# Kernel optimization log

Hardware: AMD Instinct MI355X
Metric: run time of the kernel (lower is better)

Reference implementation:

```python
import jax, jax.numpy as jnp
import numpy as np

N_NODES = 20000
N_EDGES = 200000
C = 64             # channel multiplicity (hidden_irreps = 64x0e + 64x1o)
LMAX = 3
NLM = (LMAX + 1) ** 2   # 16 spherical-harmonic components
NUM_ELEM = 10
R_DIM = 8          # radial embedding out dim
MLP_H = 64
AVG_NEI = 10.0
L_OF_LM = np.repeat(np.arange(LMAX + 1), 2 * np.arange(LMAX + 1) + 1)  # [16] l index per lm slot


def setup_inputs() -> dict:
    key = jax.random.key(0)
    k = jax.random.split(key, 16)
    f32 = jnp.float32
    elems = jax.random.randint(k[0], (N_NODES,), 0, NUM_ELEM)
    one_hot = jax.nn.one_hot(elems, NUM_ELEM, dtype=f32)
    node_features = jax.random.normal(k[1], (N_NODES, C), dtype=f32)
    angular_embedding = jax.random.normal(k[2], (N_EDGES, NLM), dtype=f32)
    radial_embedding = jax.random.normal(k[3], (N_EDGES, R_DIM), dtype=f32)
    edge_index = jax.random.randint(k[4], (2, N_EDGES), 0, N_NODES)

    def w(kk, shape, fan_in):  # e3nn-style 1/sqrt(fan_in) normalization baked into init
        return jax.random.normal(kk, shape, dtype=f32) / float(np.sqrt(fan_in))

    W_up = w(k[5], (C, C), C)
    W_mlp1 = w(k[6], (R_DIM, MLP_H), R_DIM)
    W_mlp2 = w(k[7], (MLP_H, MLP_H), MLP_H)
    W_mlp3 = w(k[8], (MLP_H, MLP_H), MLP_H)
    W_mlp4 = w(k[9], (MLP_H, (LMAX + 1) * C), MLP_H)
    W_lin = w(k[10], (LMAX + 1, C, C), C)
    W_skip = w(k[11], (C, NUM_ELEM, C), C * NUM_ELEM)
    W_c0 = jax.random.normal(k[12], (NUM_ELEM, C), dtype=f32)
    W_c1 = jax.random.normal(k[13], (NUM_ELEM, C), dtype=f32)
    W_p0 = w(k[14], (C, C), C)
    W_p1 = w(k[15], (C, C), C)
    return dict(node_features=node_features, one_hot=one_hot,
                angular_embedding=angular_embedding, radial_embedding=radial_embedding,
                W_up=W_up, W_mlp1=W_mlp1, W_mlp2=W_mlp2, W_mlp3=W_mlp3, W_mlp4=W_mlp4,
                W_lin=W_lin, W_skip=W_skip, W_c0=W_c0, W_c1=W_c1, W_p0=W_p0, W_p1=W_p1,
                edge_index=edge_index)


def reference(node_features, one_hot, angular_embedding, radial_embedding,
              W_up, W_mlp1, W_mlp2, W_mlp3, W_mlp4, W_lin, W_skip,
              W_c0, W_c1, W_p0, W_p1, edge_index):
    sender, receiver = edge_index[0], edge_index[1]
    n = node_features.shape[0]
    # ---- interaction block (RealAgnosticResidual; node feats are pure scalars 64x0e) ----
    x = node_features @ W_up                                    # linear_up [N,C]
    h = jax.nn.silu(radial_embedding @ W_mlp1)                  # radial MLP -> per-edge TP weights
    h = jax.nn.silu(h @ W_mlp2)
    h = jax.nn.silu(h @ W_mlp3)
    tp_w = (h @ W_mlp4).reshape(-1, LMAX + 1, C)                # [E,4,C] (one weight per l path, uvu)
    w_lm = tp_w[:, L_OF_LM, :]                                  # [E,16,C]
    # uvu tensor product of 0e node feats with spherical harmonics (CG trivial for 0e x l -> l)
    msg = x[sender][:, None, :] * angular_embedding[:, :, None] * w_lm   # [E,16,C]
    agg = jax.ops.segment_sum(msg, receiver, num_segments=n) / AVG_NEI   # scatter-sum [N,16,C]
    feats = jnp.einsum('nmc,mck->nmk', agg, W_lin[L_OF_LM])     # per-l channel-mixing linear [N,16,C]
    # residual skip FCTP(64x0e, 10x0e -> hidden): only the 0e block is connected
    sc0 = jnp.einsum('nc,na,cak->nk', node_features, one_hot, W_skip)    # [N,C]
    # ---- equivariant product basis block (correlation = 1) ----
    wn0 = one_hot @ W_c0                                        # element-dependent weights [N,C]
    wn1 = one_hot @ W_c1
    f0 = feats[:, 0, :] * wn0                                   # l=0 output [N,C]
    f1 = feats[:, 1:4, :] * wn1[:, None, :]                     # l=1 output [N,3,C]
    out0 = f0 @ W_p0 + sc0                                      # [N,C]
    out1 = jnp.einsum('nmc,ck->nmk', f1, W_p1)                  # [N,3,C] (sc 1o block is zero)
    # flatten to e3nn channel-major irreps layout -> node_env [N, C*(1+3)]
    return jnp.concatenate([out0, jnp.swapaxes(out1, 1, 2).reshape(n, -1)], axis=-1)
```

## Files before the change

### kernel.cpp

```cpp
#include <hip/hip_runtime.h>

typedef __attribute__((ext_vector_type(8))) short s16x8;
typedef __attribute__((ext_vector_type(4))) float f32x4;

__device__ inline float bf2f(ushort u) {
    union { unsigned int i; float f; } v; v.i = ((unsigned)u) << 16; return v.f;
}
__device__ inline float u2f(unsigned u) {
    union { unsigned int i; float f; } v; v.i = u; return v.f;
}
__device__ inline ushort f2bf(float f) {
    union { float f; unsigned int i; } v; v.f = f;
    unsigned r = v.i + 0x7FFFu + ((v.i >> 16) & 1u);
    return (ushort)(r >> 16);
}
__device__ inline unsigned cvt_pk(float lo, float hi) {
    unsigned d;
    asm("v_cvt_pk_bf16_f32 %0, %1, %2" : "=v"(d) : "v"(lo), "v"(hi));
    return d;
}
__device__ inline float silu_f(float x) {
    float e;
    asm("v_exp_f32 %0, %1" : "=v"(e) : "v"(x * -1.44269504f));
    float d = 1.f + e, r;
    asm("v_rcp_f32 %0, %1" : "=v"(r) : "v"(d));
    return x * r;
}

__global__ __launch_bounds__(256) void prep_up_kernel(
    const float* __restrict__ nf, const float* __restrict__ W_up,
    ushort* __restrict__ x_ws,
    const float* __restrict__ W1, const float* __restrict__ W2,
    const float* __restrict__ W3, const float* __restrict__ W4,
    const float* __restrict__ W_lin, const float* __restrict__ Wp0,
    const float* __restrict__ Wp1, const float* __restrict__ W_skip,
    ushort* __restrict__ wimg, int* __restrict__ counts, int N) {
    __shared__ float sW[64 * 64];
    __shared__ float sNf[32][64];
    int tid = threadIdx.x;
    int nub = N / 32;
    if ((int)blockIdx.x < nub) {
        size_t n0 = (size_t)blockIdx.x * 32;
        for (int i = tid; i < 4096; i += 256) sW[i] = W_up[i];
        for (int i = tid; i < 2048; i += 256) {
            int r = i >> 6, c = i & 63;
            sNf[r][c] = nf[(n0 + r) * 64 + c];
        }
        __syncthreads();
        int r = tid >> 3, k0 = (tid & 7) * 8;
        float acc[8] = {0, 0, 0, 0, 0, 0, 0, 0};
        #pragma unroll 4
        for (int c = 0; c < 64; ++c) {
            float v = sNf[r][c];
            const float* wr = &sW[c * 64 + k0];
            #pragma unroll
            for (int j = 0; j < 8; ++j) acc[j] += v * wr[j];
        }
        uint4 val;
        val.x = cvt_pk(acc[0], acc[1]);
        val.y = cvt_pk(acc[2], acc[3]);
        val.z = cvt_pk(acc[4], acc[5]);
        val.w = cvt_pk(acc[6], acc[7]);
        *(uint4*)(x_ws + (n0 + r) * 64 + k0) = val;
        return;
    }
    int idx = ((int)blockIdx.x - nub) * 256 + tid;
    if (idx < N) counts[idx] = 0;
    if (idx < 4096) {
        int m = idx >> 6, k = idx & 63;
        int dst = m * 64 + ((((k >> 3) ^ (m & 7))) << 3) + (k & 7);
        wimg[dst] = (k < 8) ? f2bf(W1[k * 64 + m]) : (ushort)0;
    } else if (idx < 8192) {
        int i = idx - 4096;
        int m = i >> 6, k = i & 63;
        int dst = 4096 + m * 64 + ((((k >> 3) ^ (m & 7))) << 3) + (k & 7);
        wimg[dst] = f2bf(W2[k * 64 + m]);
    } else if (idx < 12288) {
        int i = idx - 8192;
        int m = i >> 6, k = i & 63;
        int dst = 8192 + m * 64 + ((((k >> 3) ^ (m & 7))) << 3) + (k & 7);
        wimg[dst] = f2bf(W3[k * 64 + m]);
    } else if (idx < 20480) {
        int i = idx - 12288;
        int m = i >> 6, k = i & 63;
        int dst = 12288 + m * 64 + ((((k >> 3) ^ (m & 7))) << 3) + (k & 7);
        wimg[dst] = f2bf(W4[k * 256 + m]);
    } else if (idx < 29696) {
        int i = idx - 20480;
        int row = i / 72, k = i % 72;
        int l = row >> 6, col = row & 63;
        wimg[idx] = (k < 64) ? f2bf(W_lin[l * 4096 + k * 64 + col]) : (ushort)0;
    } else if (idx < 38912) {
        int i = idx - 29696;
        int row = i / 72, k = i % 72;
        int l = row >> 6, col = row & 63;
        const float* Wp = l ? Wp1 : Wp0;
        wimg[idx] = (k < 64) ? f2bf(Wp[k * 64 + col]) : (ushort)0;
    } else if (idx < 79872) {
        int i = idx - 38912;
        wimg[idx] = f2bf(W_skip[i]);
    }
}

__global__ __launch_bounds__(256) void hist_kernel(const int* __restrict__ recv,
                                                   int* __restrict__ counts, int E) {
    int e = blockIdx.x * 256 + threadIdx.x;
    if (e < E) atomicAdd(&counts[recv[e]], 1);
}

__global__ __launch_bounds__(1024) void scan_kernel(const int* __restrict__ counts,
                                                    int* __restrict__ offsets,
                                                    int* __restrict__ cursor, int n) {
    __shared__ int wsums[16];
    int tid = threadIdx.x, lane = tid & 63, wid = tid >> 6;
    int CH = (n + 1023) >> 10;
    int base = tid * CH;
    int cnt[20];
    int tot = 0;
    if (CH <= 20) {
        #pragma unroll
        for (int j = 0; j < 20; ++j) {
            int i = base + j;
            cnt[j] = (j < CH && i < n) ? counts[i] : 0;
            tot += cnt[j];
        }
    } else {
        for (int j = 0; j < CH; ++j) {
            int i = base + j;
            if (i < n) tot += counts[i];
        }
    }
    int v = tot;
    for (int off = 1; off < 64; off <<= 1) {
        int t = __shfl_up(v, off, 64);
        if (lane >= off) v += t;
    }
    if (lane == 63) wsums[wid] = v;
    __syncthreads();
    if (tid == 0) {
        int acc = 0;
        for (int w = 0; w < 16; ++w) { int t = wsums[w]; wsums[w] = acc; acc += t; }
    }
    __syncthreads();
    int excl = wsums[wid] + v - tot;
    if (CH <= 20) {
        #pragma unroll
        for (int j = 0; j < 20; ++j) {
            int i = base + j;
            if (j < CH && i < n) {
                offsets[i] = excl; cursor[i] = excl; excl += cnt[j];
            }
        }
    } else {
        for (int j = 0; j < CH; ++j) {
            int i = base + j;
            if (i < n) { offsets[i] = excl; cursor[i] = excl; excl += counts[i]; }
        }
    }
    if (tid == 1023) offsets[n] = excl;
}

__global__ __launch_bounds__(256) void edge_mlp_kernel(
    const int* __restrict__ recv, const int* __restrict__ sender,
    const float* __restrict__ angular, const float* __restrict__ radial,
    int* __restrict__ cursor, int* __restrict__ csr_sender,
    float4* __restrict__ csr_ang, const ushort* __restrict__ wimg,
    unsigned* __restrict__ tpw32, int E) {
    __shared__ __align__(16) ushort sW4[8192];
    __shared__ __align__(16) ushort sB[4][1024];
    int tid = threadIdx.x, lane = tid & 63, wave = tid >> 6;
    int n = lane & 15, hi = lane >> 4;

    for (int i = tid; i < 1024; i += 256)
        ((s16x8*)sW4)[i] = ((const s16x8*)(wimg + 12288))[i];

    s16x8 w1f[4], w2f[4][2], w3f[4][2];
    #pragma unroll
    for (int mt = 0; mt < 4; ++mt) {
        int row = mt * 16 + n, r7 = row & 7;
        w1f[mt] = *(const s16x8*)(wimg + row * 64 + ((hi ^ r7) << 3));
        #pragma unroll
        for (int ks = 0; ks < 2; ++ks) {
            w2f[mt][ks] = *(const s16x8*)(wimg + 4096 + row * 64 + (((ks * 4 + hi) ^ r7) << 3));
            w3f[mt][ks] = *(const s16x8*)(wimg + 8192 + row * 64 + (((ks * 4 + hi) ^ r7) << 3));
        }
    }
    __syncthreads();

    char* myB = (char*)sB[wave];
    int n7 = n & 7;

    for (int sub = 0; sub < 2; ++sub) {
        int base = blockIdx.x * 128 + wave * 32 + sub * 16;
        if (base >= E) break;
        int e = base + n;
        bool oke = e < E;
        int eC = min(e, E - 1);

        s16x8 bR;
        #pragma unroll
        for (int j = 0; j < 8; ++j) bR[j] = 0;
        int pos = 0;
        if (hi == 0) {
            float4 r0 = *(const float4*)(radial + (size_t)eC * 8);
            float4 r1 = *(const float4*)(radial + (size_t)eC * 8 + 4);
            union { s16x8 v; uint4 u; } bb;
            bb.u.x = cvt_pk(r0.x, r0.y);
            bb.u.y = cvt_pk(r0.z, r0.w);
            bb.u.z = cvt_pk(r1.x, r1.y);
            bb.u.w = cvt_pk(r1.z, r1.w);
            bR = bb.v;
            if (oke) {
                int r = recv[e];
                pos = atomicAdd(&cursor[r], 1);
                csr_sender[pos] = sender[e];
                csr_ang[pos] = *(const float4*)(angular + (size_t)e * 16);
            }
        }
        pos = __shfl(pos, n);

        f32x4 zero = {0.f, 0.f, 0.f, 0.f};
        f32x4 d[4];
        #pragma unroll
        for (int mt = 0; mt < 4; ++mt)
            d[mt] = __builtin_amdgcn_mfma_f32_16x16x32_bf16(w1f[mt], bR, zero, 0, 0, 0);

        #pragma unroll
        for (int mt = 0; mt < 4; ++mt) {
            uint2 val = {cvt_pk(silu_f(d[mt][0]), silu_f(d[mt][1])),
                         cvt_pk(silu_f(d[mt][2]), silu_f(d[mt][3]))};
            int slot = mt * 2 + (hi >> 1);
            *(uint2*)(myB + n * 128 + ((slot ^ n7) << 4) + (hi & 1) * 8) = val;
        }
        s16x8 b0 = *(const s16x8*)(myB + n * 128 + ((hi ^ n7) << 4));
        s16x8 b1 = *(const s16x8*)(myB + n * 128 + (((4 + hi) ^ n7) << 4));

        #pragma unroll
        for (int mt = 0; mt < 4; ++mt) {
            d[mt] = __builtin_amdgcn_mfma_f32_16x16x32_bf16(w2f[mt][0], b0, zero, 0, 0, 0);
            d[mt] = __builtin_amdgcn_mfma_f32_16x16x32_bf16(w2f[mt][1], b1, d[mt], 0, 0, 0);
        }
        #pragma unroll
        for (int mt = 0; mt < 4; ++mt) {
            uint2 val = {cvt_pk(silu_f(d[mt][0]), silu_f(d[mt][1])),
                         cvt_pk(silu_f(d[mt][2]), silu_f(d[mt][3]))};
            int slot = mt * 2 + (hi >> 1);
            *(uint2*)(myB + n * 128 + ((slot ^ n7) << 4) + (hi & 1) * 8) = val;
        }
        b0 = *(const s16x8*)(myB + n * 128 + ((hi ^ n7) << 4));
        b1 = *(const s16x8*)(myB + n * 128 + (((4 + hi) ^ n7) << 4));

        #pragma unroll
        for (int mt = 0; mt < 4; ++mt) {
            d[mt] = __builtin_amdgcn_mfma_f32_16x16x32_bf16(w3f[mt][0], b0, zero, 0, 0, 0);
            d[mt] = __builtin_amdgcn_mfma_f32_16x16x32_bf16(w3f[mt][1], b1, d[mt], 0, 0, 0);
        }
        #pragma unroll
        for (int mt = 0; mt < 4; ++mt) {
            uint2 val = {cvt_pk(silu_f(d[mt][0]), silu_f(d[mt][1])),
                         cvt_pk(silu_f(d[mt][2]), silu_f(d[mt][3]))};
            int slot = mt * 2 + (hi >> 1);
            *(uint2*)(myB + n * 128 + ((slot ^ n7) << 4) + (hi & 1) * 8) = val;
        }
        b0 = *(const s16x8*)(myB + n * 128 + ((hi ^ n7) << 4));
        b1 = *(const s16x8*)(myB + n * 128 + (((4 + hi) ^ n7) << 4));

        f32x4 o[8];
        #pragma unroll
        for (int mt = 0; mt < 8; ++mt) {
            int row = mt * 16 + n, r7 = row & 7;
            s16x8 a0f = *(const s16x8*)(sW4 + row * 64 + ((hi ^ r7) << 3));
            s16x8 a1f = *(const s16x8*)(sW4 + row * 64 + (((4 + hi) ^ r7) << 3));
            o[mt] = __builtin_amdgcn_mfma_f32_16x16x32_bf16(a0f, b0, zero, 0, 0, 0);
            o[mt] = __builtin_amdgcn_mfma_f32_16x16x32_bf16(a1f, b1, o[mt], 0, 0, 0);
        }
        if (oke) {
            size_t rowbase = (size_t)pos * 64;
            #pragma unroll
            for (int mt = 0; mt < 4; ++mt) {
                uint4 val;
                val.x = cvt_pk(o[mt][0], o[mt + 4][0]);
                val.y = cvt_pk(o[mt][1], o[mt + 4][1]);
                val.z = cvt_pk(o[mt][2], o[mt + 4][2]);
                val.w = cvt_pk(o[mt][3], o[mt + 4][3]);
                *(uint4*)(tpw32 + rowbase + mt * 16 + hi * 4) = val;
            }
        }
    }
}

__global__ __launch_bounds__(256) void agg_kernel(const float4* __restrict__ csr_ang,
                                                  const int* __restrict__ csr_sender,
                                                  const unsigned* __restrict__ tpw32,
                                                  const int* __restrict__ offsets,
                                                  const ushort* __restrict__ x_ws,
                                                  ushort* __restrict__ agg, int N) {
    int wave = threadIdx.x >> 6, lane = threadIdx.x & 63;
    int node = blockIdx.x * 4 + wave;
    if (node >= N) return;
    int beg = offsets[node], end = offsets[node + 1];
    float a0 = 0, a1 = 0, a2 = 0, a3 = 0;
    for (int cb = beg; cb < end; cb += 64) {
        int m = min(64, end - cb);
        int sv = csr_sender[cb + min(lane, m - 1)];
        for (int e0 = 0; e0 < m; e0 += 4) {
            unsigned t[4];
            ushort x[4];
            float4 g[4];
            #pragma unroll
            for (int j = 0; j < 4; ++j) {
                int e = e0 + j;
                int ec = min(e, m - 1);
                t[j] = tpw32[(size_t)(cb + ec) * 64 + lane];
                x[j] = x_ws[(size_t)__shfl(sv, ec) * 64 + lane];
                if (e < m) g[j] = csr_ang[cb + e];
                else g[j] = make_float4(0.f, 0.f, 0.f, 0.f);
            }
            #pragma unroll
            for (int j = 0; j < 4; ++j) {
                float xv = bf2f(x[j]);
                float tp0 = u2f(t[j] << 16);
                float tp1 = u2f(t[j] & 0xffff0000u);
                float y0 = xv * tp0, y1 = xv * tp1;
                a0 += g[j].x * y0;
                a1 += g[j].y * y1;
                a2 += g[j].z * y1;
                a3 += g[j].w * y1;
            }
        }
    }
    size_t b = (size_t)node * 256 + lane;
    agg[b] = f2bf(a0 * 0.1f);
    agg[b + 64] = f2bf(a1 * 0.1f);
    agg[b + 128] = f2bf(a2 * 0.1f);
    agg[b + 192] = f2bf(a3 * 0.1f);
}

__global__ __launch_bounds__(256) void node_out2_kernel(
    const float* __restrict__ nf, const float* __restrict__ one_hot,
    const ushort* __restrict__ wimg, const float* __restrict__ W_c0,
    const float* __restrict__ W_c1, const ushort* __restrict__ agg,
    float* __restrict__ out) {
    __shared__ __align__(16) ushort sWl[2 * 64 * 72];
    __shared__ __align__(16) ushort sF[4][32 * 72];
    __shared__ float sSc[32][64];
    __shared__ float sWc[2][640];
    __shared__ int sElem[32];
    int tid = threadIdx.x;
    int n0 = blockIdx.x * 32;
    int lane = tid & 63, m = tid >> 6;
    int lsel = (m == 0) ? 0 : 1;

    s16x8 pf[4][2];
    #pragma unroll
    for (int nt = 0; nt < 4; ++nt)
        #pragma unroll
        for (int ks = 0; ks < 2; ++ks)
            pf[nt][ks] = *(const s16x8*)(wimg + 29696 +
                (lsel * 64 + nt * 16 + (lane & 15)) * 72 + ks * 32 + (lane >> 4) * 8);

    for (int i = tid; i < 1152; i += 256)
        ((s16x8*)sWl)[i] = ((const s16x8*)(wimg + 20480))[i];
    for (int i = tid; i < 1280; i += 256)
        sWc[i >= 640][i % 640] = (i >= 640 ? W_c1 : W_c0)[i % 640];
    if (tid < 32) {
        int nn = n0 + tid, e = 0;
        for (int a = 0; a < 10; ++a)
            if (one_hot[(size_t)nn * 10 + a] > 0.5f) { e = a; break; }
        sElem[tid] = e;
    }
    __syncthreads();

    {
        int nl = tid >> 3, k0 = (tid & 7) * 8;
        int nn = n0 + nl, elem = sElem[nl];
        float acc[8] = {0, 0, 0, 0, 0, 0, 0, 0};
        const ushort* wskb = wimg + 38912;
        for (int c = 0; c < 64; ++c) {
            float v = nf[(size_t)nn * 64 + c];
            s16x8 w = *(const s16x8*)(wskb + ((size_t)c * 10 + elem) * 64 + k0);
            #pragma unroll
            for (int j = 0; j < 8; ++j) acc[j] += v * bf2f((ushort)w[j]);
        }
        #pragma unroll
        for (int j = 0; j < 8; ++j) sSc[nl][k0 + j] = acc[j];
    }

    f32x4 acc[2][4] = {};
    s16x8 afr[2][2];
    #pragma unroll
    for (int mt = 0; mt < 2; ++mt)
        #pragma unroll
        for (int ks = 0; ks < 2; ++ks)
            afr[mt][ks] = *(const s16x8*)(agg +
                (((size_t)(n0 + mt * 16 + (lane & 15))) * 4 + m) * 64 +
                ks * 32 + (lane >> 4) * 8);
    #pragma unroll
    for (int nt = 0; nt < 4; ++nt)
        #pragma unroll
        for (int ks = 0; ks < 2; ++ks) {
            s16x8 b = *(const s16x8*)(sWl + (lsel * 64 + nt * 16 + (lane & 15)) * 72 +
                                      ks * 32 + (lane >> 4) * 8);
            #pragma unroll
            for (int mt = 0; mt < 2; ++mt)
                acc[mt][nt] = __builtin_amdgcn_mfma_f32_16x16x32_bf16(afr[mt][ks], b,
                                                                      acc[mt][nt], 0, 0, 0);
        }

    #pragma unroll
    for (int mt = 0; mt < 2; ++mt)
        #pragma unroll
        for (int nt = 0; nt < 4; ++nt)
            #pragma unroll
            for (int r = 0; r < 4; ++r) {
                int nl = mt * 16 + (lane >> 4) * 4 + r;
                int k = nt * 16 + (lane & 15);
                float scale = sWc[lsel][sElem[nl] * 64 + k];
                sF[m][nl * 72 + k] = f2bf(acc[mt][nt][r] * scale);
            }
    __syncthreads();

    f32x4 acc2[2][4] = {};
    s16x8 af2[2][2];
    #pragma unroll
    for (int mt = 0; mt < 2; ++mt)
        #pragma unroll
        for (int ks = 0; ks < 2; ++ks)
            af2[mt][ks] = *(const s16x8*)(&sF[m][(mt * 16 + (lane & 15)) * 72 +
                                                 ks * 32 + (lane >> 4) * 8]);
    #pragma unroll
    for (int nt = 0; nt < 4; ++nt)
        #pragma unroll
        for (int ks = 0; ks < 2; ++ks) {
            #pragma unroll
            for (int mt = 0; mt < 2; ++mt)
                acc2[mt][nt] = __builtin_amdgcn_mfma_f32_16x16x32_bf16(af2[mt][ks],
                                                                       pf[nt][ks],
                                                                       acc2[mt][nt], 0, 0, 0);
        }

    #pragma unroll
    for (int mt = 0; mt < 2; ++mt)
        #pragma unroll
        for (int nt = 0; nt < 4; ++nt)
            #pragma unroll
            for (int r = 0; r < 4; ++r) {
                int nl = mt * 16 + (lane >> 4) * 4 + r;
                int k = nt * 16 + (lane & 15);
                size_t nn = (size_t)n0 + nl;
                if (m == 0)
                    out[nn * 256 + k] = acc2[mt][nt][r] + sSc[nl][k];
                else
                    out[nn * 256 + 64 + k * 3 + (m - 1)] = acc2[mt][nt][r];
            }
}

extern "C" void kernel_launch(void* const* d_in, const int* in_sizes, int n_in,
                              void* d_out, int out_size, void* d_ws, size_t ws_size,
                              hipStream_t stream) {
    const float* node_features = (const float*)d_in[0];
    const float* one_hot = (const float*)d_in[1];
    const float* angular = (const float*)d_in[2];
    const float* radial = (const float*)d_in[3];
    const float* W_up = (const float*)d_in[4];
    const float* W_mlp1 = (const float*)d_in[5];
    const float* W_mlp2 = (const float*)d_in[6];
    const float* W_mlp3 = (const float*)d_in[7];
    const float* W_mlp4 = (const float*)d_in[8];
    const float* W_lin = (const float*)d_in[9];
    const float* W_skip = (const float*)d_in[10];
    const float* W_c0 = (const float*)d_in[11];
    const float* W_c1 = (const float*)d_in[12];
    const float* W_p0 = (const float*)d_in[13];
    const float* W_p1 = (const float*)d_in[14];
    const int* edge_index = (const int*)d_in[15];
    float* out = (float*)d_out;

    int N = in_sizes[0] / 64;
    int E = in_sizes[2] / 16;
    const int* sender = edge_index;
    const int* receiver = edge_index + E;

    char* p = (char*)d_ws;
    ushort* x_ws = (ushort*)p;      p += (size_t)N * 64 * 2;
    unsigned* tpw32 = (unsigned*)p; p += (size_t)E * 64 * 4;
    ushort* agg = (ushort*)p;       p += (size_t)N * 256 * 2;
    ushort* wimg = (ushort*)p;      p += 79872 * 2;
    float4* csr_ang = (float4*)p;   p += (size_t)E * 16;
    int* counts = (int*)p;          p += (size_t)N * 4;
    int* offsets = (int*)p;         p += (size_t)(N + 1) * 4;
    int* cursor = (int*)p;          p += (size_t)N * 4;
    int* csr_sender = (int*)p;      p += (size_t)E * 4;

    prep_up_kernel<<<N / 32 + 312, 256, 0, stream>>>(node_features, W_up, x_ws,
                                                     W_mlp1, W_mlp2, W_mlp3, W_mlp4,
                                                     W_lin, W_p0, W_p1, W_skip, wimg,
                                                     counts, N);
    hist_kernel<<<(E + 255) / 256, 256, 0, stream>>>(receiver, counts, E);
    scan_kernel<<<1, 1024, 0, stream>>>(counts, offsets, cursor, N);
    edge_mlp_kernel<<<(E + 127) / 128, 256, 0, stream>>>(receiver, sender, angular,
                                                         radial, cursor, csr_sender,
                                                         csr_ang, wimg, tpw32, E);
    agg_kernel<<<(N + 3) / 4, 256, 0, stream>>>(csr_ang, csr_sender, tpw32, offsets,
                                                x_ws, agg, N);
    node_out2_kernel<<<N / 32, 256, 0, stream>>>(node_features, one_hot, wimg,
                                                 W_c0, W_c1, agg, out);
}
```

Before: 117.6 us.

## Write edge MLP output in edge order and gather via CSR edge-id indirection

The edge MLP kernel now writes each edge's radial weights at its original edge index, not at the CSR position, and records only the edge id in the CSR array. It no longer copies sender ids and angular data into CSR order. The aggregation kernel reads sender, angular and the weight row indirectly through the edge id. This removes the scattered copy writes and makes the large weight store coalesced, at the cost of random-access reads of weights and angular data during aggregation. It also splits the final MFMA loop into pairs to cut register pressure.

```diff
diff --git a/kernel.cpp b/kernel.cpp
--- a/kernel.cpp
+++ b/kernel.cpp
@@ -161,11 +161,9 @@
 }
 
 __global__ __launch_bounds__(256) void edge_mlp_kernel(
-    const int* __restrict__ recv, const int* __restrict__ sender,
-    const float* __restrict__ angular, const float* __restrict__ radial,
-    int* __restrict__ cursor, int* __restrict__ csr_sender,
-    float4* __restrict__ csr_ang, const ushort* __restrict__ wimg,
-    unsigned* __restrict__ tpw32, int E) {
+    const int* __restrict__ recv, const float* __restrict__ radial,
+    int* __restrict__ cursor, int* __restrict__ csr_eid,
+    const ushort* __restrict__ wimg, unsigned* __restrict__ tpw32, int E) {
     __shared__ __align__(16) ushort sW4[8192];
     __shared__ __align__(16) ushort sB[4][1024];
     int tid = threadIdx.x, lane = tid & 63, wave = tid >> 6;
@@ -200,7 +198,6 @@
         s16x8 bR;
         #pragma unroll
         for (int j = 0; j < 8; ++j) bR[j] = 0;
-        int pos = 0;
         if (hi == 0) {
             float4 r0 = *(const float4*)(radial + (size_t)eC * 8);
             float4 r1 = *(const float4*)(radial + (size_t)eC * 8 + 4);
@@ -211,13 +208,10 @@
             bb.u.w = cvt_pk(r1.z, r1.w);
             bR = bb.v;
             if (oke) {
-                int r = recv[e];
-                pos = atomicAdd(&cursor[r], 1);
-                csr_sender[pos] = sender[e];
-                csr_ang[pos] = *(const float4*)(angular + (size_t)e * 16);
-            }
-        }
-        pos = __shfl(pos, n);
+                int pos = atomicAdd(&cursor[recv[e]], 1);
+                csr_eid[pos] = e;
+            }
+        }
 
         f32x4 zero = {0.f, 0.f, 0.f, 0.f};
         f32x4 d[4];
@@ -265,32 +259,34 @@
         b0 = *(const s16x8*)(myB + n * 128 + ((hi ^ n7) << 4));
         b1 = *(const s16x8*)(myB + n * 128 + (((4 + hi) ^ n7) << 4));
 
-        f32x4 o[8];
-        #pragma unroll
-        for (int mt = 0; mt < 8; ++mt) {
-            int row = mt * 16 + n, r7 = row & 7;
-            s16x8 a0f = *(const s16x8*)(sW4 + row * 64 + ((hi ^ r7) << 3));
-            s16x8 a1f = *(const s16x8*)(sW4 + row * 64 + (((4 + hi) ^ r7) << 3));
-            o[mt] = __builtin_amdgcn_mfma_f32_16x16x32_bf16(a0f, b0, zero, 0, 0, 0);
-            o[mt] = __builtin_amdgcn_mfma_f32_16x16x32_bf16(a1f, b1, o[mt], 0, 0, 0);
-        }
-        if (oke) {
-            size_t rowbase = (size_t)pos * 64;
-            #pragma unroll
-            for (int mt = 0; mt < 4; ++mt) {
+        size_t rowbase = (size_t)e * 64;
+        #pragma unroll
+        for (int mt = 0; mt < 4; ++mt) {
+            int row0 = mt * 16 + n, r70 = row0 & 7;
+            int row1 = (mt + 4) * 16 + n, r71 = row1 & 7;
+            s16x8 a0lo = *(const s16x8*)(sW4 + row0 * 64 + ((hi ^ r70) << 3));
+            s16x8 a1lo = *(const s16x8*)(sW4 + row0 * 64 + (((4 + hi) ^ r70) << 3));
+            s16x8 a0hi = *(const s16x8*)(sW4 + row1 * 64 + ((hi ^ r71) << 3));
+            s16x8 a1hi = *(const s16x8*)(sW4 + row1 * 64 + (((4 + hi) ^ r71) << 3));
+            f32x4 olo = __builtin_amdgcn_mfma_f32_16x16x32_bf16(a0lo, b0, zero, 0, 0, 0);
+            olo = __builtin_amdgcn_mfma_f32_16x16x32_bf16(a1lo, b1, olo, 0, 0, 0);
+            f32x4 ohi = __builtin_amdgcn_mfma_f32_16x16x32_bf16(a0hi, b0, zero, 0, 0, 0);
+            ohi = __builtin_amdgcn_mfma_f32_16x16x32_bf16(a1hi, b1, ohi, 0, 0, 0);
+            if (oke) {
                 uint4 val;
-                val.x = cvt_pk(o[mt][0], o[mt + 4][0]);
-                val.y = cvt_pk(o[mt][1], o[mt + 4][1]);
-                val.z = cvt_pk(o[mt][2], o[mt + 4][2]);
-                val.w = cvt_pk(o[mt][3], o[mt + 4][3]);
+                val.x = cvt_pk(olo[0], ohi[0]);
+                val.y = cvt_pk(olo[1], ohi[1]);
+                val.z = cvt_pk(olo[2], ohi[2]);
+                val.w = cvt_pk(olo[3], ohi[3]);
                 *(uint4*)(tpw32 + rowbase + mt * 16 + hi * 4) = val;
             }
         }
     }
 }
 
-__global__ __launch_bounds__(256) void agg_kernel(const float4* __restrict__ csr_ang,
-                                                  const int* __restrict__ csr_sender,
+__global__ __launch_bounds__(256) void agg_kernel(const float* __restrict__ angular,
+                                                  const int* __restrict__ sender,
+                                                  const int* __restrict__ csr_eid,
                                                   const unsigned* __restrict__ tpw32,
                                                   const int* __restrict__ offsets,
                                                   const ushort* __restrict__ x_ws,
@@ -302,7 +298,8 @@
     float a0 = 0, a1 = 0, a2 = 0, a3 = 0;
     for (int cb = beg; cb < end; cb += 64) {
         int m = min(64, end - cb);
-        int sv = csr_sender[cb + min(lane, m - 1)];
+        int ev = csr_eid[cb + min(lane, m - 1)];
+        int sv = sender[ev];
         for (int e0 = 0; e0 < m; e0 += 4) {
             unsigned t[4];
             ushort x[4];
@@ -311,9 +308,10 @@
             for (int j = 0; j < 4; ++j) {
                 int e = e0 + j;
                 int ec = min(e, m - 1);
-                t[j] = tpw32[(size_t)(cb + ec) * 64 + lane];
+                int eidj = __shfl(ev, ec);
+                t[j] = tpw32[(size_t)eidj * 64 + lane];
                 x[j] = x_ws[(size_t)__shfl(sv, ec) * 64 + lane];
-                if (e < m) g[j] = csr_ang[cb + e];
+                if (e < m) g[j] = *(const float4*)(angular + (size_t)eidj * 16);
                 else g[j] = make_float4(0.f, 0.f, 0.f, 0.f);
             }
             #pragma unroll
@@ -486,11 +484,10 @@
     unsigned* tpw32 = (unsigned*)p; p += (size_t)E * 64 * 4;
     ushort* agg = (ushort*)p;       p += (size_t)N * 256 * 2;
     ushort* wimg = (ushort*)p;      p += 79872 * 2;
-    float4* csr_ang = (float4*)p;   p += (size_t)E * 16;
     int* counts = (int*)p;          p += (size_t)N * 4;
     int* offsets = (int*)p;         p += (size_t)(N + 1) * 4;
     int* cursor = (int*)p;          p += (size_t)N * 4;
-    int* csr_sender = (int*)p;      p += (size_t)E * 4;
+    int* csr_eid = (int*)p;         p += (size_t)E * 4;
 
     prep_up_kernel<<<N / 32 + 312, 256, 0, stream>>>(node_features, W_up, x_ws,
                                                      W_mlp1, W_mlp2, W_mlp3, W_mlp4,
@@ -498,11 +495,10 @@
                                                      counts, N);
     hist_kernel<<<(E + 255) / 256, 256, 0, stream>>>(receiver, counts, E);
     scan_kernel<<<1, 1024, 0, stream>>>(counts, offsets, cursor, N);
-    edge_mlp_kernel<<<(E + 127) / 128, 256, 0, stream>>>(receiver, sender, angular,
-                                                         radial, cursor, csr_sender,
-                                                         csr_ang, wimg, tpw32, E);
-    agg_kernel<<<(N + 3) / 4, 256, 0, stream>>>(csr_ang, csr_sender, tpw32, offsets,
-                                                x_ws, agg, N);
+    edge_mlp_kernel<<<(E + 127) / 128, 256, 0, stream>>>(receiver, radial, cursor,
+                                                         csr_eid, wimg, tpw32, E);
+    agg_kernel<<<(N + 3) / 4, 256, 0, stream>>>(angular, sender, csr_eid, tpw32,
+                                                offsets, x_ws, agg, N);
     node_out2_kernel<<<N / 32, 256, 0, stream>>>(node_features, one_hot, wimg,
                                                  W_c0, W_c1, agg, out);
 }
```

New measurement: 120.0 us. 2.0% more time.
